# Performance work log

Hardware: AMD Instinct MI355X
Metric: run time of the kernel (lower is better)

## Reference

```python
import jax, jax.numpy as jnp
import numpy as np

STATE_DIM = 4        # per-block state size (rel pos + rel vel, 2D)
N_NEIGH = 64         # neighbors per agent
BATCH = 4096         # observations in the batch (len(x) in torch code)
PHI_H, PHI_OUT = 256, 64
RHO_H, ACTION_DIM = 256, 2
R_AGENT = 0.15
A_MAX = 2.0


def setup_inputs() -> dict:
    key = jax.random.key(0)
    ks = jax.random.split(key, 5)

    def w(k, i, o):
        return jax.random.normal(k, (i, o), jnp.float32) / np.sqrt(i).astype(np.float32)

    x = jax.random.normal(ks[0], (BATCH, (N_NEIGH + 2) * STATE_DIM), jnp.float32)
    return dict(
        x=x,
        phi_w1=w(ks[1], STATE_DIM, PHI_H), phi_b1=jnp.zeros((PHI_H,), jnp.float32),
        phi_w2=w(ks[2], PHI_H, PHI_OUT), phi_b2=jnp.zeros((PHI_OUT,), jnp.float32),
        rho_w1=w(ks[3], PHI_OUT, RHO_H), rho_b1=jnp.zeros((RHO_H,), jnp.float32),
        rho_w2=w(ks[4], RHO_H, ACTION_DIM), rho_b2=jnp.zeros((ACTION_DIM,), jnp.float32),
    )


def reference(x, phi_w1, phi_b1, phi_w2, phi_b2, rho_w1, rho_b1, rho_w2, rho_b2):
    B = x.shape[0]
    blocks = x.reshape(B, -1, STATE_DIM)                 # [B, n_n+2, sd]
    # DeepSet: phi per block, permutation-invariant sum, rho head.
    h = jax.nn.relu(jnp.einsum('bns,sh->bnh', blocks, phi_w1) + phi_b1)
    phi = jnp.einsum('bnh,ho->bno', h, phi_w2) + phi_b2  # [B, n_n+2, phi_out]
    X = phi.sum(axis=1)                                  # [B, phi_out]
    h2 = jax.nn.relu(X @ rho_w1 + rho_b1)
    a = A_MAX * jnp.tanh(h2 @ rho_w2 + rho_b2)           # [B, action_dim]
    # Barrier: neighbor blocks start at block index 2; take first half (positions).
    p = blocks[:, 2:, : STATE_DIM // 2]                  # [B, n_n, 2]
    d = jnp.linalg.norm(p, axis=-1, keepdims=True)       # [B, n_n, 1]
    barrier = jnp.sum(-p / (d - R_AGENT) ** 2, axis=1)   # [B, 2]
    barrier = jax.lax.stop_gradient(barrier)  # torch goes through numpy -> detached
    a = a + barrier
    scale = A_MAX / jnp.max(a)  # torch.max(a_max)/torch.max(a_wbarrier), global max
    return jnp.where(scale < 1.0, a * scale, a)
```

## Files before the change

kernel.cpp:

```cpp
#include <hip/hip_runtime.h>
#include <math.h>


#define GROWS 8
#define NBLOCKS (4096 / GROWS)

__device__ __forceinline__ unsigned fkey(float f) {
    unsigned u = __float_as_uint(f);
    return (u & 0x80000000u) ? ~u : (u | 0x80000000u);
}
__device__ __forceinline__ float fkey_inv(unsigned k) {
    return __uint_as_float((k & 0x80000000u) ? (k & 0x7fffffffu) : ~k);
}

__global__ __launch_bounds__(256) void barrier_net_main(
    const float* __restrict__ x,
    const float* __restrict__ w1,  const float* __restrict__ b1,
    const float* __restrict__ w2,  const float* __restrict__ b2,
    const float* __restrict__ rw1, const float* __restrict__ rb1,
    const float* __restrict__ rw2, const float* __restrict__ rb2,
    float* __restrict__ out, unsigned* __restrict__ maxkey)
{
    __shared__ float sx[GROWS][264];
    __shared__ float sH[GROWS][256];
    __shared__ float sX[GROWS][64];
    __shared__ float sh2[GROWS][256];
    __shared__ float sbar[GROWS][2];
    __shared__ float sa[GROWS * 2];

    const int tid  = threadIdx.x;
    const int lane = tid & 63;
    const int wv   = tid >> 6;
    const int b0   = blockIdx.x * GROWS;

    for (int i = tid; i < GROWS * 264; i += 256) {
        int r = i / 264, c = i % 264;
        sx[r][c] = x[(b0 + r) * 264 + c];
    }
    __syncthreads();

    float w[4];
    w[0] = w1[tid]; w[1] = w1[256 + tid]; w[2] = w1[512 + tid]; w[3] = w1[768 + tid];
    const float bias = b1[tid];
    for (int r = 0; r < GROWS; r++) {
        float acc = 0.f;
        #pragma unroll
        for (int n = 0; n < 66; n++) {
            float h = bias;
            h = fmaf(sx[r][n * 4 + 0], w[0], h);
            h = fmaf(sx[r][n * 4 + 1], w[1], h);
            h = fmaf(sx[r][n * 4 + 2], w[2], h);
            h = fmaf(sx[r][n * 4 + 3], w[3], h);
            acc += fmaxf(h, 0.f);
        }
        sH[r][tid] = acc;
    }

    #pragma unroll
    for (int rr = 0; rr < 2; rr++) {
        int r = wv * 2 + rr;
        float px = sx[r][(lane + 2) * 4 + 0];
        float py = sx[r][(lane + 2) * 4 + 1];
        float d  = sqrtf(px * px + py * py);
        float t  = d - 0.15f;
        float inv = 1.0f / (t * t);
        float bx = -px * inv, by = -py * inv;
        #pragma unroll
        for (int m = 32; m >= 1; m >>= 1) {
            bx += __shfl_xor(bx, m);
            by += __shfl_xor(by, m);
        }
        if (lane == 0) { sbar[r][0] = bx; sbar[r][1] = by; }
    }
    __syncthreads();

    {
        const int o  = tid & 63;
        const int rg = tid >> 6;
        float a0 = 0.f, a1 = 0.f;
        #pragma unroll 8
        for (int k = 0; k < 256; k++) {
            float wk = w2[k * 64 + o];
            a0 = fmaf(sH[rg * 2 + 0][k], wk, a0);
            a1 = fmaf(sH[rg * 2 + 1][k], wk, a1);
        }
        float bb = 66.0f * b2[o];
        sX[rg * 2 + 0][o] = a0 + bb;
        sX[rg * 2 + 1][o] = a1 + bb;
    }
    __syncthreads();

    {
        float acc3[GROWS];
        #pragma unroll
        for (int r = 0; r < GROWS; r++) acc3[r] = rb1[tid];
        for (int o4 = 0; o4 < 16; o4++) {
            float wv3[4];
            #pragma unroll
            for (int j = 0; j < 4; j++) wv3[j] = rw1[(o4 * 4 + j) * 256 + tid];
            #pragma unroll
            for (int r = 0; r < GROWS; r++) {
                float4 xv = ((const float4*)sX[r])[o4];
                acc3[r] = fmaf(xv.x, wv3[0], acc3[r]);
                acc3[r] = fmaf(xv.y, wv3[1], acc3[r]);
                acc3[r] = fmaf(xv.z, wv3[2], acc3[r]);
                acc3[r] = fmaf(xv.w, wv3[3], acc3[r]);
            }
        }
        #pragma unroll
        for (int r = 0; r < GROWS; r++) sh2[r][tid] = fmaxf(acc3[r], 0.f);
    }
    __syncthreads();

    {
        const int grp = tid >> 5;
        const int gl  = tid & 31;
        float p0 = 0.f, p1 = 0.f;
        const float2* rw2v = (const float2*)rw2;
        #pragma unroll
        for (int i = 0; i < 8; i++) {
            int j = gl + 32 * i;
            float  h  = sh2[grp][j];
            float2 wk = rw2v[j];
            p0 = fmaf(h, wk.x, p0);
            p1 = fmaf(h, wk.y, p1);
        }
        #pragma unroll
        for (int m = 16; m >= 1; m >>= 1) {
            p0 += __shfl_xor(p0, m);
            p1 += __shfl_xor(p1, m);
        }
        if (gl == 0) {
            float a0 = 2.0f * tanhf(p0 + rb2[0]) + sbar[grp][0];
            float a1 = 2.0f * tanhf(p1 + rb2[1]) + sbar[grp][1];
            out[(b0 + grp) * 2 + 0] = a0;
            out[(b0 + grp) * 2 + 1] = a1;
            sa[grp * 2 + 0] = a0;
            sa[grp * 2 + 1] = a1;
        }
    }
    __syncthreads();

    if (tid == 0) {
        float m = sa[0];
        #pragma unroll
        for (int i = 1; i < GROWS * 2; i++) m = fmaxf(m, sa[i]);
        atomicMax(maxkey, fkey(m));
    }
}

__global__ __launch_bounds__(256) void barrier_net_scale(
    float* __restrict__ out, const unsigned* __restrict__ maxkey)
{
    int i = blockIdx.x * 256 + threadIdx.x;
    float amax  = fkey_inv(*maxkey);
    float scale = 2.0f / amax;
    float a = out[i];
    out[i] = (scale < 1.0f) ? a * scale : a;
}

extern "C" void kernel_launch(void* const* d_in, const int* in_sizes, int n_in,
                              void* d_out, int out_size, void* d_ws, size_t ws_size,
                              hipStream_t stream) {
    const float* x   = (const float*)d_in[0];
    const float* w1  = (const float*)d_in[1];
    const float* b1  = (const float*)d_in[2];
    const float* w2  = (const float*)d_in[3];
    const float* b2  = (const float*)d_in[4];
    const float* rw1 = (const float*)d_in[5];
    const float* rb1 = (const float*)d_in[6];
    const float* rw2 = (const float*)d_in[7];
    const float* rb2 = (const float*)d_in[8];
    float* out = (float*)d_out;
    unsigned* maxkey = (unsigned*)d_ws;

    hipMemsetAsync(d_ws, 0, 4, stream);
    barrier_net_main<<<NBLOCKS, 256, 0, stream>>>(
        x, w1, b1, w2, b2, rw1, rb1, rw2, rb2, out, maxkey);
    barrier_net_scale<<<8192 / 256, 256, 0, stream>>>(out, maxkey);
}
```

Baseline: 103.8 us.

## Restructure DeepSet kernel: wave-per-row phi, readlane broadcasts, fewer rows per block

```diff
diff --git a/kernel.cpp b/kernel.cpp
--- a/kernel.cpp
+++ b/kernel.cpp
@@ -2,7 +2,7 @@
 #include <math.h>
 
 
-#define GROWS 8
+#define GROWS 4
 #define NBLOCKS (4096 / GROWS)
 
 __device__ __forceinline__ unsigned fkey(float f) {
@@ -12,8 +12,11 @@
 __device__ __forceinline__ float fkey_inv(unsigned k) {
     return __uint_as_float((k & 0x80000000u) ? (k & 0x7fffffffu) : ~k);
 }
+__device__ __forceinline__ float rlane(float v, int i) {
+    return __uint_as_float(__builtin_amdgcn_readlane(__float_as_uint(v), i));
+}
 
-__global__ __launch_bounds__(256) void barrier_net_main(
+__global__ __launch_bounds__(256, 4) void barrier_net_main(
     const float* __restrict__ x,
     const float* __restrict__ w1,  const float* __restrict__ b1,
     const float* __restrict__ w2,  const float* __restrict__ b2,
@@ -21,46 +24,45 @@
     const float* __restrict__ rw2, const float* __restrict__ rb2,
     float* __restrict__ out, unsigned* __restrict__ maxkey)
 {
-    __shared__ float sx[GROWS][264];
-    __shared__ float sH[GROWS][256];
-    __shared__ float sX[GROWS][64];
-    __shared__ float sh2[GROWS][256];
+    __shared__ float sH[GROWS][264];
+    __shared__ float sXp[4][GROWS][68];
+    __shared__ float sP4[4][GROWS][2];
     __shared__ float sbar[GROWS][2];
     __shared__ float sa[GROWS * 2];
 
-    const int tid  = threadIdx.x;
-    const int lane = tid & 63;
-    const int wv   = tid >> 6;
-    const int b0   = blockIdx.x * GROWS;
+    const int tid = threadIdx.x;
+    const int ln  = tid & 63;
+    const int wv  = tid >> 6;
+    const int b0  = blockIdx.x * GROWS;
+    const int row = __builtin_amdgcn_readfirstlane(b0 + wv);
+    const float4* __restrict__ x4 = (const float4*)(x + (size_t)row * 264);
 
-    for (int i = tid; i < GROWS * 264; i += 256) {
-        int r = i / 264, c = i % 264;
-        sx[r][c] = x[(b0 + r) * 264 + c];
+    float4 w1r0 = ((const float4*)(w1      ))[ln];
+    float4 w1r1 = ((const float4*)(w1 + 256))[ln];
+    float4 w1r2 = ((const float4*)(w1 + 512))[ln];
+    float4 w1r3 = ((const float4*)(w1 + 768))[ln];
+    float4 b1r  = ((const float4*)b1)[ln];
+    float a0 = 0.f, a1 = 0.f, a2 = 0.f, a3 = 0.f;
+    #pragma unroll 6
+    for (int n = 0; n < 66; n++) {
+        float4 xv = x4[n];
+        float h0 = b1r.x, h1 = b1r.y, h2 = b1r.z, h3 = b1r.w;
+        h0 = fmaf(xv.x, w1r0.x, h0); h1 = fmaf(xv.x, w1r0.y, h1);
+        h2 = fmaf(xv.x, w1r0.z, h2); h3 = fmaf(xv.x, w1r0.w, h3);
+        h0 = fmaf(xv.y, w1r1.x, h0); h1 = fmaf(xv.y, w1r1.y, h1);
+        h2 = fmaf(xv.y, w1r1.z, h2); h3 = fmaf(xv.y, w1r1.w, h3);
+        h0 = fmaf(xv.z, w1r2.x, h0); h1 = fmaf(xv.z, w1r2.y, h1);
+        h2 = fmaf(xv.z, w1r2.z, h2); h3 = fmaf(xv.z, w1r2.w, h3);
+        h0 = fmaf(xv.w, w1r3.x, h0); h1 = fmaf(xv.w, w1r3.y, h1);
+        h2 = fmaf(xv.w, w1r3.z, h2); h3 = fmaf(xv.w, w1r3.w, h3);
+        a0 += fmaxf(h0, 0.f); a1 += fmaxf(h1, 0.f);
+        a2 += fmaxf(h2, 0.f); a3 += fmaxf(h3, 0.f);
     }
-    __syncthreads();
+    ((float4*)sH[wv])[ln] = make_float4(a0, a1, a2, a3);
 
-    float w[4];
-    w[0] = w1[tid]; w[1] = w1[256 + tid]; w[2] = w1[512 + tid]; w[3] = w1[768 + tid];
-    const float bias = b1[tid];
-    for (int r = 0; r < GROWS; r++) {
-        float acc = 0.f;
-        #pragma unroll
-        for (int n = 0; n < 66; n++) {
-            float h = bias;
-            h = fmaf(sx[r][n * 4 + 0], w[0], h);
-            h = fmaf(sx[r][n * 4 + 1], w[1], h);
-            h = fmaf(sx[r][n * 4 + 2], w[2], h);
-            h = fmaf(sx[r][n * 4 + 3], w[3], h);
-            acc += fmaxf(h, 0.f);
-        }
-        sH[r][tid] = acc;
-    }
-
-    #pragma unroll
-    for (int rr = 0; rr < 2; rr++) {
-        int r = wv * 2 + rr;
-        float px = sx[r][(lane + 2) * 4 + 0];
-        float py = sx[r][(lane + 2) * 4 + 1];
+    {
+        float4 pv = x4[ln + 2];
+        float px = pv.x, py = pv.y;
         float d  = sqrtf(px * px + py * py);
         float t  = d - 0.15f;
         float inv = 1.0f / (t * t);
@@ -70,77 +72,79 @@
             bx += __shfl_xor(bx, m);
             by += __shfl_xor(by, m);
         }
-        if (lane == 0) { sbar[r][0] = bx; sbar[r][1] = by; }
+        if (ln == 0) { sbar[wv][0] = bx; sbar[wv][1] = by; }
     }
     __syncthreads();
 
+    float Hq0 = sH[0][(wv << 6) + ln];
+    float Hq1 = sH[1][(wv << 6) + ln];
+    float Hq2 = sH[2][(wv << 6) + ln];
+    float Hq3 = sH[3][(wv << 6) + ln];
     {
-        const int o  = tid & 63;
-        const int rg = tid >> 6;
-        float a0 = 0.f, a1 = 0.f;
-        #pragma unroll 8
-        for (int k = 0; k < 256; k++) {
-            float wk = w2[k * 64 + o];
-            a0 = fmaf(sH[rg * 2 + 0][k], wk, a0);
-            a1 = fmaf(sH[rg * 2 + 1][k], wk, a1);
+        float xp0 = 0.f, xp1 = 0.f, xp2 = 0.f, xp3 = 0.f;
+        const float* w2q = w2 + (wv << 12);
+        #pragma unroll 16
+        for (int i = 0; i < 64; i++) {
+            float wv2 = w2q[(i << 6) + ln];
+            xp0 = fmaf(rlane(Hq0, i), wv2, xp0);
+            xp1 = fmaf(rlane(Hq1, i), wv2, xp1);
+            xp2 = fmaf(rlane(Hq2, i), wv2, xp2);
+            xp3 = fmaf(rlane(Hq3, i), wv2, xp3);
         }
-        float bb = 66.0f * b2[o];
-        sX[rg * 2 + 0][o] = a0 + bb;
-        sX[rg * 2 + 1][o] = a1 + bb;
+        sXp[wv][0][ln] = xp0; sXp[wv][1][ln] = xp1;
+        sXp[wv][2][ln] = xp2; sXp[wv][3][ln] = xp3;
     }
     __syncthreads();
 
-    {
-        float acc3[GROWS];
-        #pragma unroll
-        for (int r = 0; r < GROWS; r++) acc3[r] = rb1[tid];
-        for (int o4 = 0; o4 < 16; o4++) {
-            float wv3[4];
-            #pragma unroll
-            for (int j = 0; j < 4; j++) wv3[j] = rw1[(o4 * 4 + j) * 256 + tid];
-            #pragma unroll
-            for (int r = 0; r < GROWS; r++) {
-                float4 xv = ((const float4*)sX[r])[o4];
-                acc3[r] = fmaf(xv.x, wv3[0], acc3[r]);
-                acc3[r] = fmaf(xv.y, wv3[1], acc3[r]);
-                acc3[r] = fmaf(xv.z, wv3[2], acc3[r]);
-                acc3[r] = fmaf(xv.w, wv3[3], acc3[r]);
-            }
-        }
-        #pragma unroll
-        for (int r = 0; r < GROWS; r++) sh2[r][tid] = fmaxf(acc3[r], 0.f);
+    float bb = 66.0f * b2[ln];
+    float Xf0 = sXp[0][0][ln] + sXp[1][0][ln] + sXp[2][0][ln] + sXp[3][0][ln] + bb;
+    float Xf1 = sXp[0][1][ln] + sXp[1][1][ln] + sXp[2][1][ln] + sXp[3][1][ln] + bb;
+    float Xf2 = sXp[0][2][ln] + sXp[1][2][ln] + sXp[2][2][ln] + sXp[3][2][ln] + bb;
+    float Xf3 = sXp[0][3][ln] + sXp[1][3][ln] + sXp[2][3][ln] + sXp[3][3][ln] + bb;
+
+    float c0, c1, c2, c3;
+    c0 = c1 = c2 = c3 = rb1[tid];
+    #pragma unroll 16
+    for (int i = 0; i < 64; i++) {
+        float rwv = rw1[(i << 8) + tid];
+        c0 = fmaf(rlane(Xf0, i), rwv, c0);
+        c1 = fmaf(rlane(Xf1, i), rwv, c1);
+        c2 = fmaf(rlane(Xf2, i), rwv, c2);
+        c3 = fmaf(rlane(Xf3, i), rwv, c3);
     }
-    __syncthreads();
+    c0 = fmaxf(c0, 0.f); c1 = fmaxf(c1, 0.f);
+    c2 = fmaxf(c2, 0.f); c3 = fmaxf(c3, 0.f);
 
     {
-        const int grp = tid >> 5;
-        const int gl  = tid & 31;
-        float p0 = 0.f, p1 = 0.f;
-        const float2* rw2v = (const float2*)rw2;
+        float2 r2 = ((const float2*)rw2)[tid];
+        float p00 = c0 * r2.x, p01 = c0 * r2.y;
+        float p10 = c1 * r2.x, p11 = c1 * r2.y;
+        float p20 = c2 * r2.x, p21 = c2 * r2.y;
+        float p30 = c3 * r2.x, p31 = c3 * r2.y;
         #pragma unroll
-        for (int i = 0; i < 8; i++) {
-            int j = gl + 32 * i;
-            float  h  = sh2[grp][j];
-            float2 wk = rw2v[j];
-            p0 = fmaf(h, wk.x, p0);
-            p1 = fmaf(h, wk.y, p1);
+        for (int m = 32; m >= 1; m >>= 1) {
+            p00 += __shfl_xor(p00, m); p01 += __shfl_xor(p01, m);
+            p10 += __shfl_xor(p10, m); p11 += __shfl_xor(p11, m);
+            p20 += __shfl_xor(p20, m); p21 += __shfl_xor(p21, m);
+            p30 += __shfl_xor(p30, m); p31 += __shfl_xor(p31, m);
         }
-        #pragma unroll
-        for (int m = 16; m >= 1; m >>= 1) {
-            p0 += __shfl_xor(p0, m);
-            p1 += __shfl_xor(p1, m);
-        }
-        if (gl == 0) {
-            float a0 = 2.0f * tanhf(p0 + rb2[0]) + sbar[grp][0];
-            float a1 = 2.0f * tanhf(p1 + rb2[1]) + sbar[grp][1];
-            out[(b0 + grp) * 2 + 0] = a0;
-            out[(b0 + grp) * 2 + 1] = a1;
-            sa[grp * 2 + 0] = a0;
-            sa[grp * 2 + 1] = a1;
+        if (ln == 0) {
+            sP4[wv][0][0] = p00; sP4[wv][0][1] = p01;
+            sP4[wv][1][0] = p10; sP4[wv][1][1] = p11;
+            sP4[wv][2][0] = p20; sP4[wv][2][1] = p21;
+            sP4[wv][3][0] = p30; sP4[wv][3][1] = p31;
         }
     }
     __syncthreads();
 
+    if (tid < GROWS * 2) {
+        int r = tid >> 1, c = tid & 1;
+        float pre = sP4[0][r][c] + sP4[1][r][c] + sP4[2][r][c] + sP4[3][r][c] + rb2[c];
+        float a = 2.0f * tanhf(pre) + sbar[r][c];
+        out[(b0 + r) * 2 + c] = a;
+        sa[tid] = a;
+    }
+    __syncthreads();
     if (tid == 0) {
         float m = sa[0];
         #pragma unroll
```

New measurement: 98.68 us. 4.9% less time.
